# Performance work log

Hardware: AMD Instinct MI355X
Metric: run time of the kernel (lower is better)

Reference implementation:

```python
import jax, jax.numpy as jnp
import numpy as np

HEAD_DIM = 128


def _apply_rotary(x, cos, sin):
    # x: [B, S, H, HD]; cos/sin: [S, HD//2]
    xr = x.reshape(*x.shape[:-1], -1, 2)  # interleaved pairs
    xe, xo = xr[..., 0], xr[..., 1]
    c = cos[None, :, None, :]
    s = sin[None, :, None, :]
    oe = xe * c - xo * s
    oo = xe * s + xo * c
    return jnp.stack([oe, oo], axis=-1).reshape(x.shape)


def setup_inputs() -> dict:
    key = jax.random.key(0)
    ks = jax.random.split(key, 8)
    B, S, D = 2, 1024, 4096
    KVD = 1024  # n_kv_heads * head_dim = 8 * 128
    MAXB, MAXS, KVH, HD = 2, 2048, 8, HEAD_DIM
    theta = 500000.0
    # rotary tables (real/imag of freqs_cis)
    inv = 1.0 / theta ** (np.arange(0, HD, 2)[: HD // 2].astype(np.float32) / HD)
    t = np.arange(S, dtype=np.float32)
    fr = np.outer(t, inv)
    sc = 0.02
    return {
        "x": jax.random.normal(ks[0], (B, S, D), jnp.float32),
        "wq": jax.random.normal(ks[1], (D, D), jnp.float32) * sc,
        "wk": jax.random.normal(ks[2], (D, KVD), jnp.float32) * sc,
        "wv": jax.random.normal(ks[3], (D, KVD), jnp.float32) * sc,
        "wo": jax.random.normal(ks[4], (D, D), jnp.float32) * sc,
        "freqs_cos": jnp.asarray(np.cos(fr)),
        "freqs_sin": jnp.asarray(np.sin(fr)),
        "cache_k": jnp.zeros((MAXB, MAXS, KVH, HD), jnp.float32),
        "cache_v": jnp.zeros((MAXB, MAXS, KVH, HD), jnp.float32),
        "start_pos": 0,
    }


def reference(x, wq, wk, wv, wo, freqs_cos, freqs_sin, cache_k, cache_v, start_pos):
    B, S, D = x.shape
    HD = HEAD_DIM
    H = wq.shape[1] // HD
    KVH = wk.shape[1] // HD
    n_rep = H // KVH

    xq = (x @ wq).reshape(B, S, H, HD)
    xk = (x @ wk).reshape(B, S, KVH, HD)
    xv = (x @ wv).reshape(B, S, KVH, HD)

    xq = _apply_rotary(xq, freqs_cos, freqs_sin)
    xk = _apply_rotary(xk, freqs_cos, freqs_sin)

    # KV-cache update (scatter at start_pos), then read back prefix
    cache_k = cache_k.at[:B, start_pos:start_pos + S].set(xk)
    cache_v = cache_v.at[:B, start_pos:start_pos + S].set(xv)
    keys = cache_k[:B, : start_pos + S]    # [B, T, KVH, HD]
    values = cache_v[:B, : start_pos + S]

    # GQA: repeat kv heads
    keys = jnp.repeat(keys, n_rep, axis=2)      # [B, T, H, HD]
    values = jnp.repeat(values, n_rep, axis=2)

    scale = 1.0 / jnp.sqrt(jnp.float32(HD))
    scores = jnp.einsum("bshd,bthd->bhst", xq, keys) * scale  # [B, H, S, T]

    # causal mask: zeros for the start_pos prefix, upper-triangular -inf after
    T = start_pos + S
    causal = jnp.triu(jnp.full((S, S), -jnp.inf, jnp.float32), k=1)
    mask = jnp.concatenate([jnp.zeros((S, start_pos), jnp.float32), causal], axis=1)  # [S, T]
    scores = scores + mask[None, None, :, :]

    probs = jax.nn.softmax(scores, axis=-1)
    out = jnp.einsum("bhst,bthd->bshd", probs, values).reshape(B, S, D)
    return out @ wo
```

## Files before the change

kernel.cpp:

```cpp
#include <hip/hip_runtime.h>
#include <stdint.h>

#define B_    2
#define S_    1024
#define D_    4096
#define KVD_  1024
#define H_    32
#define KVH_  8
#define HD_   128
#define M_    (B_ * S_)
#define N1_   (D_ + 2 * KVD_)
#define QK_SCALE_L2E (0.08838834764831845f * 1.4426950408889634f)

typedef __attribute__((ext_vector_type(8))) short bf16x8;
typedef __attribute__((ext_vector_type(4))) float f32x4;
typedef __attribute__((ext_vector_type(4))) unsigned short u16x4;
typedef __attribute__((ext_vector_type(8))) unsigned short u16x8;

__device__ inline unsigned short f2bf(float f) {
  unsigned u = __float_as_uint(f);
  u += 0x7FFFu + ((u >> 16) & 1u);
  return (unsigned short)(u >> 16);
}
__device__ inline float bf2f(unsigned short b) {
  return __uint_as_float(((unsigned)b) << 16);
}

#define ASYNC_LD16(g, l) __builtin_amdgcn_global_load_lds( \
    (const __attribute__((address_space(1))) void*)(g),    \
    (__attribute__((address_space(3))) void*)(l), 16, 0, 0)

#define MFMA16(a, b, c) __builtin_amdgcn_mfma_f32_16x16x32_bf16(a, b, c, 0, 0, 0)

#define WAIT_LGKM0() do { asm volatile("s_waitcnt lgkmcnt(0)" ::: "memory"); \
                          __builtin_amdgcn_sched_barrier(0); } while (0)
#define SCHED_PIN() __builtin_amdgcn_sched_barrier(0)
#define BAR() __builtin_amdgcn_s_barrier()

__global__ __launch_bounds__(256) void k_cvt_x(const float* __restrict__ x,
                                               unsigned short* __restrict__ xb) {
  size_t i = ((size_t)blockIdx.x * 256 + threadIdx.x) * 4;
  float4 v = *(const float4*)(x + i);
  u16x4 o;
  o[0] = f2bf(v.x); o[1] = f2bf(v.y); o[2] = f2bf(v.z); o[3] = f2bf(v.w);
  *(u16x4*)(xb + i) = o;
}

__global__ __launch_bounds__(256) void k_transpose_w(const float* __restrict__ in,
                                                     unsigned short* __restrict__ out,
                                                     int R, int C) {
  __shared__ unsigned short tile[64][72];
  int t = threadIdx.x;
  int c0 = blockIdx.x * 64, r0 = blockIdx.y * 64;
#pragma unroll
  for (int j = 0; j < 4; ++j) {
    int r = (t >> 4) + 16 * j;
    int c = (t & 15) * 4;
    float4 v = *(const float4*)(in + (size_t)(r0 + r) * C + c0 + c);
    tile[r][c + 0] = f2bf(v.x); tile[r][c + 1] = f2bf(v.y);
    tile[r][c + 2] = f2bf(v.z); tile[r][c + 3] = f2bf(v.w);
  }
  __syncthreads();
#pragma unroll
  for (int j = 0; j < 2; ++j) {
    int cc = (t >> 3) + 32 * j;
    int r = (t & 7) * 8;
    u16x8 o;
#pragma unroll
    for (int i = 0; i < 8; ++i) o[i] = tile[r + i][cc];
    *(u16x8*)(out + (size_t)(c0 + cc) * R + r0 + r) = o;
  }
}

__global__ __launch_bounds__(512, 2) void k_gemm_g1(const unsigned short* __restrict__ A,
                                                    const unsigned short* __restrict__ Bt,
                                                    unsigned short* __restrict__ C) {
  __shared__ unsigned short L[2 * 28672];
  const int tid = threadIdx.x, lane = tid & 63, w = tid >> 6;
  const int l15 = lane & 15, l4 = lane >> 4;
  const int wm = w >> 2, wn = w & 3;
  const int brow = blockIdx.y * 256, bcol = blockIdx.x * 192;
  const unsigned short* gA = A + (size_t)brow * 4096;
  const unsigned short* gB = Bt + (size_t)bcol * 4096;
  const int srow = lane >> 3;
  const int scol = ((lane & 7) ^ (srow & 7)) * 8;

#define G1_ST_A(buf, kt, r0) ASYNC_LD16( \
    gA + (size_t)((r0) + w * 8 + srow) * 4096 + (kt) * 64 + scol, \
    L + (buf) * 28672 + ((r0) + w * 8) * 64)
#define G1_ST_B(buf, kt, r0) ASYNC_LD16( \
    gB + (size_t)((r0) + w * 8 + srow) * 4096 + (kt) * 64 + scol, \
    L + (buf) * 28672 + 16384 + ((r0) + w * 8) * 64)
#define G1_ST_TILE(buf, kt) do { \
    G1_ST_A(buf, kt, 0); G1_ST_A(buf, kt, 64); G1_ST_A(buf, kt, 128); G1_ST_A(buf, kt, 192); \
    G1_ST_B(buf, kt, 0); G1_ST_B(buf, kt, 64); G1_ST_B(buf, kt, 128); } while (0)

  const int aoff0 = (wm * 128 + l15) * 64 + ((l4 + 0) ^ (l15 & 7)) * 8;
  const int aoff1 = (wm * 128 + l15) * 64 + ((l4 + 4) ^ (l15 & 7)) * 8;
  const int boff0 = 16384 + (wn * 48 + l15) * 64 + ((l4 + 0) ^ (l15 & 7)) * 8;
  const int boff1 = 16384 + (wn * 48 + l15) * 64 + ((l4 + 4) ^ (l15 & 7)) * 8;

  f32x4 acc[8][3] = {};

  G1_ST_TILE(0, 0);
  G1_ST_TILE(1, 1);
  asm volatile("s_waitcnt vmcnt(7)" ::: "memory");
  BAR();

  for (int t = 0; t < 64; ++t) {
    const unsigned short* Lc = L + (t & 1) * 28672;
    bf16x8 af[4], bk[3];

#pragma unroll
    for (int m = 0; m < 4; ++m) af[m] = *(const bf16x8*)(Lc + aoff0 + m * 1024);
#pragma unroll
    for (int n = 0; n < 3; ++n) bk[n] = *(const bf16x8*)(Lc + boff0 + n * 1024);
    SCHED_PIN(); BAR(); WAIT_LGKM0();
    __builtin_amdgcn_s_setprio(1);
#pragma unroll
    for (int m = 0; m < 4; ++m)
#pragma unroll
      for (int n = 0; n < 3; ++n) acc[m][n] = MFMA16(af[m], bk[n], acc[m][n]);
    __builtin_amdgcn_s_setprio(0);
    BAR();

#pragma unroll
    for (int m = 0; m < 4; ++m) af[m] = *(const bf16x8*)(Lc + aoff0 + (m + 4) * 1024);
    SCHED_PIN(); BAR(); WAIT_LGKM0();
    __builtin_amdgcn_s_setprio(1);
#pragma unroll
    for (int m = 0; m < 4; ++m)
#pragma unroll
      for (int n = 0; n < 3; ++n) acc[m + 4][n] = MFMA16(af[m], bk[n], acc[m + 4][n]);
    __builtin_amdgcn_s_setprio(0);
    BAR();

#pragma unroll
    for (int m = 0; m < 4; ++m) af[m] = *(const bf16x8*)(Lc + aoff1 + m * 1024);
#pragma unroll
    for (int n = 0; n < 3; ++n) bk[n] = *(const bf16x8*)(Lc + boff1 + n * 1024);
    SCHED_PIN(); BAR(); WAIT_LGKM0();
    __builtin_amdgcn_s_setprio(1);
#pragma unroll
    for (int m = 0; m < 4; ++m)
#pragma unroll
      for (int n = 0; n < 3; ++n) acc[m][n] = MFMA16(af[m], bk[n], acc[m][n]);
    __builtin_amdgcn_s_setprio(0);
    BAR();

#pragma unroll
    for (int m = 0; m < 4; ++m) af[m] = *(const bf16x8*)(Lc + aoff1 + (m + 4) * 1024);
    SCHED_PIN(); BAR(); WAIT_LGKM0();
    __builtin_amdgcn_s_setprio(1);
#pragma unroll
    for (int m = 0; m < 4; ++m)
#pragma unroll
      for (int n = 0; n < 3; ++n) acc[m + 4][n] = MFMA16(af[m], bk[n], acc[m + 4][n]);
    __builtin_amdgcn_s_setprio(0);
    SCHED_PIN();
    if (t + 2 < 64) {
      G1_ST_TILE(t & 1, t + 2);
      asm volatile("s_waitcnt vmcnt(7)" ::: "memory");
    } else if (t + 1 < 64) {
      asm volatile("s_waitcnt vmcnt(0)" ::: "memory");
    }
    BAR();
  }
#undef G1_ST_TILE
#undef G1_ST_A
#undef G1_ST_B

#pragma unroll
  for (int mf = 0; mf < 8; ++mf)
#pragma unroll
    for (int nf = 0; nf < 3; ++nf)
#pragma unroll
      for (int q = 0; q < 4; ++q) {
        int row = brow + wm * 128 + mf * 16 + l4 * 4 + q;
        int col = bcol + wn * 48 + nf * 16 + l15;
        C[(size_t)row * N1_ + col] = f2bf(acc[mf][nf][q]);
      }
}

__global__ __launch_bounds__(512, 2) void k_gemm_g2(const unsigned short* __restrict__ A,
                                                    const unsigned short* __restrict__ Bt,
                                                    float* __restrict__ C) {
  __shared__ unsigned short L[2 * 24576];
  const int tid = threadIdx.x, lane = tid & 63, w = tid >> 6;
  const int l15 = lane & 15, l4 = lane >> 4;
  const int wm = w >> 2, wn = w & 3;
  const int brow = blockIdx.y * 128, bcol = blockIdx.x * 256;
  const unsigned short* gA = A + (size_t)brow * 4096;
  const unsigned short* gB = Bt + (size_t)bcol * 4096;
  const int srow = lane >> 3;
  const int scol = ((lane & 7) ^ (srow & 7)) * 8;

#define G2_ST_A(buf, kt, r0) ASYNC_LD16( \
    gA + (size_t)((r0) + w * 8 + srow) * 4096 + (kt) * 64 + scol, \
    L + (buf) * 24576 + ((r0) + w * 8) * 64)
#define G2_ST_B(buf, kt, r0) ASYNC_LD16( \
    gB + (size_t)((r0) + w * 8 + srow) * 4096 + (kt) * 64 + scol, \
    L + (buf) * 24576 + 8192 + ((r0) + w * 8) * 64)
#define G2_ST_TILE(buf, kt) do { \
    G2_ST_A(buf, kt, 0); G2_ST_A(buf, kt, 64); \
    G2_ST_B(buf, kt, 0); G2_ST_B(buf, kt, 64); G2_ST_B(buf, kt, 128); G2_ST_B(buf, kt, 192); } while (0)

  const int aoff0 = (wm * 64 + l15) * 64 + ((l4 + 0) ^ (l15 & 7)) * 8;
  const int aoff1 = (wm * 64 + l15) * 64 + ((l4 + 4) ^ (l15 & 7)) * 8;
  const int boff0 = 8192 + (wn * 64 + l15) * 64 + ((l4 + 0) ^ (l15 & 7)) * 8;
  const int boff1 = 8192 + (wn * 64 + l15) * 64 + ((l4 + 4) ^ (l15 & 7)) * 8;

  f32x4 acc[4][4] = {};

  G2_ST_TILE(0, 0);
  G2_ST_TILE(1, 1);
  asm volatile("s_waitcnt vmcnt(6)" ::: "memory");
  BAR();

  for (int t = 0; t < 64; ++t) {
    const unsigned short* Lc = L + (t & 1) * 24576;
    bf16x8 af[4], bk[4];

#pragma unroll
    for (int m = 0; m < 4; ++m) af[m] = *(const bf16x8*)(Lc + aoff0 + m * 1024);
#pragma unroll
    for (int n = 0; n < 4; ++n) bk[n] = *(const bf16x8*)(Lc + boff0 + n * 1024);
    SCHED_PIN(); BAR(); WAIT_LGKM0();
    __builtin_amdgcn_s_setprio(1);
#pragma unroll
    for (int m = 0; m < 4; ++m)
#pragma unroll
      for (int n = 0; n < 4; ++n) acc[m][n] = MFMA16(af[m], bk[n], acc[m][n]);
    __builtin_amdgcn_s_setprio(0);
    BAR();

#pragma unroll
    for (int m = 0; m < 4; ++m) af[m] = *(const bf16x8*)(Lc + aoff1 + m * 1024);
#pragma unroll
    for (int n = 0; n < 4; ++n) bk[n] = *(const bf16x8*)(Lc + boff1 + n * 1024);
    SCHED_PIN(); BAR(); WAIT_LGKM0();
    __builtin_amdgcn_s_setprio(1);
#pragma unroll
    for (int m = 0; m < 4; ++m)
#pragma unroll
      for (int n = 0; n < 4; ++n) acc[m][n] = MFMA16(af[m], bk[n], acc[m][n]);
    __builtin_amdgcn_s_setprio(0);
    SCHED_PIN();
    if (t + 2 < 64) {
      G2_ST_TILE(t & 1, t + 2);
      asm volatile("s_waitcnt vmcnt(6)" ::: "memory");
    } else if (t + 1 < 64) {
      asm volatile("s_waitcnt vmcnt(0)" ::: "memory");
    }
    BAR();
  }
#undef G2_ST_TILE
#undef G2_ST_A
#undef G2_ST_B

#pragma unroll
  for (int mf = 0; mf < 4; ++mf)
#pragma unroll
    for (int nf = 0; nf < 4; ++nf)
#pragma unroll
      for (int q = 0; q < 4; ++q) {
        int row = brow + wm * 64 + mf * 16 + l4 * 4 + q;
        int col = bcol + wn * 64 + nf * 16 + l15;
        C[(size_t)row * D_ + col] = acc[mf][nf][q];
      }
}

__global__ __launch_bounds__(256) void k_rope(unsigned short* __restrict__ qkv,
                                              const float* __restrict__ fc,
                                              const float* __restrict__ fs) {
  int t = blockIdx.y;
  int idx = blockIdx.x * 256 + threadIdx.x;
  int i = idx & 63;
  int hs = idx >> 6;
  int s = t & (S_ - 1);
  int n0 = (hs < H_) ? hs * HD_ : D_ + (hs - H_) * HD_;
  unsigned short* p = qkv + (size_t)t * N1_ + n0 + 2 * i;
  unsigned v = *(const unsigned*)p;
  float xe = bf2f((unsigned short)(v & 0xffff));
  float xo = bf2f((unsigned short)(v >> 16));
  float c = fc[s * 64 + i], sn = fs[s * 64 + i];
  float oe = xe * c - xo * sn;
  float oo = xe * sn + xo * c;
  if (hs < H_) { oe *= QK_SCALE_L2E; oo *= QK_SCALE_L2E; }
  *(unsigned*)p = (unsigned)f2bf(oe) | ((unsigned)f2bf(oo) << 16);
}

__global__ __launch_bounds__(256) void k_transpose_v(const unsigned short* __restrict__ qkv,
                                                     unsigned short* __restrict__ vt) {
  int bh = blockIdx.z;
  int d0 = blockIdx.x * 64;
  int s0 = blockIdx.y * 64;
  __shared__ unsigned short tile[64][72];
  int t = threadIdx.x;
  const unsigned short* src = qkv + (size_t)(bh >> 3) * S_ * N1_ + D_ + KVD_ + (bh & 7) * HD_;
#pragma unroll
  for (int j = 0; j < 2; ++j) {
    int s = (t >> 3) + 32 * j;
    int d = (t & 7) * 8;
    u16x8 v = *(const u16x8*)(src + (size_t)(s0 + s) * N1_ + d0 + d);
#pragma unroll
    for (int i = 0; i < 8; ++i) tile[s][d + i] = v[i];
  }
  __syncthreads();
#pragma unroll
  for (int j = 0; j < 2; ++j) {
    int d = (t >> 3) + 32 * j;
    int s = (t & 7) * 8;
    u16x8 o;
#pragma unroll
    for (int i = 0; i < 8; ++i) o[i] = tile[s + i][d];
    *(u16x8*)(vt + (size_t)(bh * HD_ + d0 + d) * S_ + s0 + s) = o;
  }
}

__global__ __launch_bounds__(256) void k_flash(const unsigned short* __restrict__ qkv,
                                               const unsigned short* __restrict__ vt,
                                               unsigned short* __restrict__ ao) {
  int f = blockIdx.x;
  int bh = f >> 3;
  int qt = (f & 256) ? (7 - (f & 7)) : (f & 7);
  int b = bh >> 5, h = bh & 31;
  int kh = h >> 2;
  int tid = threadIdx.x, lane = tid & 63, w = tid >> 6;
  int l15 = lane & 15, l4 = lane >> 4;

  __shared__ unsigned short Ks[2 * 64 * 128];
  __shared__ unsigned short Vs[2 * 128 * 64];
  __shared__ unsigned short Ps[4][32 * 64];

  int qb0 = qt * 128;
  int rwb = qb0 + w * 32;
  int NT = 2 * qt + 2;

  const unsigned short* qp = qkv + (size_t)(b * S_ + rwb) * N1_ + h * HD_;
  bf16x8 qf[2][4];
#pragma unroll
  for (int qr = 0; qr < 2; ++qr)
#pragma unroll
    for (int ks = 0; ks < 4; ++ks)
      qf[qr][ks] = *(const bf16x8*)(qp + (size_t)(qr * 16 + l15) * N1_ + ks * 32 + l4 * 8);

  f32x4 o[2][8];
#pragma unroll
  for (int qr = 0; qr < 2; ++qr)
#pragma unroll
    for (int d = 0; d < 8; ++d) o[qr][d] = (f32x4){0.f, 0.f, 0.f, 0.f};
  float mrun[2][4], lrun[2][4];
#pragma unroll
  for (int qr = 0; qr < 2; ++qr)
#pragma unroll
    for (int q = 0; q < 4; ++q) { mrun[qr][q] = -1e30f; lrun[qr][q] = 0.f; }

  const unsigned short* kbase = qkv + (size_t)(b * S_) * N1_ + D_ + kh * HD_;
  const unsigned short* vbase = vt + (size_t)(b * KVH_ + kh) * HD_ * S_;
  int krl = lane >> 4, kcu = lane & 15;
  int vrl = lane >> 3, vcu = lane & 7;

#define STAGE_KV(bo, itt) do {                                               \
    int kv0s = (itt) * 64;                                                   \
    _Pragma("unroll")                                                        \
    for (int j = 0; j < 4; ++j) {                                            \
      int kc = w * 4 + j;                                                    \
      int krow = kc * 4 + krl;                                               \
      int su = kcu ^ (krow & 7);                                             \
      ASYNC_LD16(kbase + (size_t)(kv0s + krow) * N1_ + su * 8,               \
                 Ks + (bo) * 8192 + kc * 512);                               \
      int vrow = kc * 8 + vrl;                                               \
      int sv = vcu ^ (vrow & 7);                                             \
      ASYNC_LD16(vbase + (size_t)vrow * S_ + kv0s + sv * 8,                  \
                 Vs + (bo) * 8192 + kc * 512);                               \
    }                                                                        \
  } while (0)

  int cur = 0;
  STAGE_KV(0, 0);

  for (int it = 0; it < NT; ++it) {
    int kv0 = it * 64;
    if (it + 1 < NT) {
      STAGE_KV(cur ^ 1, it + 1);
      asm volatile("s_waitcnt vmcnt(8)" ::: "memory");
    } else {
      asm volatile("s_waitcnt vmcnt(0)" ::: "memory");
    }
    __builtin_amdgcn_s_barrier();
    __builtin_amdgcn_sched_barrier(0);

    if (kv0 <= rwb + 31) {
      const unsigned short* Kc = Ks + cur * 8192;
      const unsigned short* Vc = Vs + cur * 8192;

      f32x4 sf[2][4] = {};
      __builtin_amdgcn_s_setprio(1);
#pragma unroll
      for (int ks = 0; ks < 4; ++ks)
#pragma unroll
        for (int n = 0; n < 4; ++n) {
          int row = n * 16 + l15;
          int u = (l4 + ks * 4) ^ (row & 7);
          bf16x8 kf = *(const bf16x8*)(Kc + row * 128 + u * 8);
          sf[0][n] = MFMA16(qf[0][ks], kf, sf[0][n]);
          sf[1][n] = MFMA16(qf[1][ks], kf, sf[1][n]);
        }
      __builtin_amdgcn_s_setprio(0);

      if (kv0 + 63 > rwb) {
#pragma unroll
        for (int qr = 0; qr < 2; ++qr)
#pragma unroll
          for (int n = 0; n < 4; ++n)
#pragma unroll
            for (int q = 0; q < 4; ++q) {
              int rq = rwb + qr * 16 + l4 * 4 + q;
              int ck = kv0 + n * 16 + l15;
              if (ck > rq) sf[qr][n][q] = -1e30f;
            }
      }

#pragma unroll
      for (int qr = 0; qr < 2; ++qr) {
        float mt[4], rs[4];
#pragma unroll
        for (int q = 0; q < 4; ++q) {
          float m0 = fmaxf(fmaxf(sf[qr][0][q], sf[qr][1][q]),
                           fmaxf(sf[qr][2][q], sf[qr][3][q]));
#pragma unroll
          for (int off = 1; off < 16; off <<= 1) m0 = fmaxf(m0, __shfl_xor(m0, off, 16));
          mt[q] = m0;
        }
        bool grow = (mt[0] > mrun[qr][0]) || (mt[1] > mrun[qr][1]) ||
                    (mt[2] > mrun[qr][2]) || (mt[3] > mrun[qr][3]);
        if (__any(grow)) {
#pragma unroll
          for (int q = 0; q < 4; ++q) {
            float mn = fmaxf(mrun[qr][q], mt[q]);
            float c = __builtin_amdgcn_exp2f(mrun[qr][q] - mn);
            lrun[qr][q] *= c;
            mrun[qr][q] = mn;
#pragma unroll
            for (int d = 0; d < 8; ++d) o[qr][d][q] *= c;
          }
        }
#pragma unroll
        for (int q = 0; q < 4; ++q) rs[q] = 0.f;
#pragma unroll
        for (int n = 0; n < 4; ++n)
#pragma unroll
          for (int q = 0; q < 4; ++q) {
            float p = __builtin_amdgcn_exp2f(sf[qr][n][q] - mrun[qr][q]);
            sf[qr][n][q] = p;
            rs[q] += p;
          }
#pragma unroll
        for (int q = 0; q < 4; ++q) {
#pragma unroll
          for (int off = 1; off < 16; off <<= 1) rs[q] += __shfl_xor(rs[q], off, 16);
          lrun[qr][q] += rs[q];
        }
      }

      unsigned short* pw = Ps[w];
#pragma unroll
      for (int qr = 0; qr < 2; ++qr)
#pragma unroll
        for (int n = 0; n < 4; ++n)
#pragma unroll
          for (int q = 0; q < 4; ++q) {
            int rp = qr * 16 + l4 * 4 + q;
            int cp = n * 16 + l15;
            pw[rp * 64 + (((cp >> 3) ^ (rp & 7)) * 8) + (cp & 7)] = f2bf(sf[qr][n][q]);
          }

      __builtin_amdgcn_s_setprio(1);
#pragma unroll
      for (int kvs = 0; kvs < 2; ++kvs) {
        bf16x8 pa0 = *(const bf16x8*)(pw + (l15) * 64 + (((l4 + kvs * 4) ^ (l15 & 7)) * 8));
        bf16x8 pa1 = *(const bf16x8*)(pw + (16 + l15) * 64 + (((l4 + kvs * 4) ^ (l15 & 7)) * 8));
#pragma unroll
        for (int d = 0; d < 8; ++d) {
          int vrow = d * 16 + l15;
          int u = (l4 + kvs * 4) ^ (vrow & 7);
          bf16x8 vf = *(const bf16x8*)(Vc + vrow * 64 + u * 8);
          o[0][d] = MFMA16(pa0, vf, o[0][d]);
          o[1][d] = MFMA16(pa1, vf, o[1][d]);
        }
      }
      __builtin_amdgcn_s_setprio(0);
    }

    __builtin_amdgcn_s_barrier();
    cur ^= 1;
  }
#undef STAGE_KV

  float invl[2][4];
#pragma unroll
  for (int qr = 0; qr < 2; ++qr)
#pragma unroll
    for (int q = 0; q < 4; ++q) invl[qr][q] = 1.f / lrun[qr][q];
#pragma unroll
  for (int qr = 0; qr < 2; ++qr)
#pragma unroll
    for (int d = 0; d < 8; ++d)
#pragma unroll
      for (int q = 0; q < 4; ++q) {
        int row = b * S_ + rwb + qr * 16 + l4 * 4 + q;
        ao[(size_t)row * D_ + h * HD_ + d * 16 + l15] = f2bf(o[qr][d][q] * invl[qr][q]);
      }
}

extern "C" void kernel_launch(void* const* d_in, const int* in_sizes, int n_in,
                              void* d_out, int out_size, void* d_ws, size_t ws_size,
                              hipStream_t stream) {
  const float* x  = (const float*)d_in[0];
  const float* wq = (const float*)d_in[1];
  const float* wk = (const float*)d_in[2];
  const float* wv = (const float*)d_in[3];
  const float* wo = (const float*)d_in[4];
  const float* fc = (const float*)d_in[5];
  const float* fs = (const float*)d_in[6];
  float* out = (float*)d_out;

  char* ws = (char*)d_ws;
  unsigned short* xb  = (unsigned short*)ws; ws += (size_t)M_ * D_ * 2;
  unsigned short* w1t = (unsigned short*)ws; ws += (size_t)N1_ * D_ * 2;
  unsigned short* wot = (unsigned short*)ws; ws += (size_t)D_ * D_ * 2;
  unsigned short* qkv = (unsigned short*)ws; ws += (size_t)M_ * N1_ * 2;
  unsigned short* vtb = (unsigned short*)ws; ws += (size_t)B_ * KVH_ * HD_ * S_ * 2;
  unsigned short* ao  = (unsigned short*)ws; ws += (size_t)M_ * D_ * 2;

  k_cvt_x<<<(M_ * D_) / 1024, 256, 0, stream>>>(x, xb);
  k_transpose_w<<<dim3(64, 64), 256, 0, stream>>>(wq, w1t, D_, D_);
  k_transpose_w<<<dim3(16, 64), 256, 0, stream>>>(wk, w1t + (size_t)D_ * D_, D_, KVD_);
  k_transpose_w<<<dim3(16, 64), 256, 0, stream>>>(wv, w1t + (size_t)(D_ + KVD_) * D_, D_, KVD_);
  k_transpose_w<<<dim3(64, 64), 256, 0, stream>>>(wo, wot, D_, D_);

  k_gemm_g1<<<dim3(N1_ / 192, M_ / 256), 512, 0, stream>>>(xb, w1t, qkv);

  k_rope<<<dim3(10, M_), 256, 0, stream>>>(qkv, fc, fs);
  k_transpose_v<<<dim3(2, 16, 16), 256, 0, stream>>>(qkv, vtb);
  k_flash<<<dim3(512), 256, 0, stream>>>(qkv, vtb, ao);

  k_gemm_g2<<<dim3(D_ / 256, M_ / 128), 512, 0, stream>>>(ao, wot, out);
}
```

Before: 309.3 us.

## Enlarge QKV GEMM tile to 256x256 with quarter-tile staged prefetch pipeline

The fused QKV projection GEMM moves from 256x192 to 256x256 block tiles, giving each wave a 128x64 sub-tile. The K-loop is restructured into eight phases per pair of K-steps, each loading a quarter-tile of LDS data. Global prefetch of the next tile is interleaved in half-tile chunks between MFMA phases instead of issued all at once. This aims to raise arithmetic intensity and spread memory traffic more evenly across compute. The trade-offs are a larger LDS footprint (128KB per block), higher register pressure, and fewer blocks in the grid.

```diff
diff --git a/kernel.cpp b/kernel.cpp
--- a/kernel.cpp
+++ b/kernel.cpp
@@ -75,109 +75,130 @@
 __global__ __launch_bounds__(512, 2) void k_gemm_g1(const unsigned short* __restrict__ A,
                                                     const unsigned short* __restrict__ Bt,
                                                     unsigned short* __restrict__ C) {
-  __shared__ unsigned short L[2 * 28672];
+  __shared__ unsigned short L[65536];
   const int tid = threadIdx.x, lane = tid & 63, w = tid >> 6;
   const int l15 = lane & 15, l4 = lane >> 4;
   const int wm = w >> 2, wn = w & 3;
-  const int brow = blockIdx.y * 256, bcol = blockIdx.x * 192;
+  const int brow = blockIdx.y * 256, bcol = blockIdx.x * 256;
   const unsigned short* gA = A + (size_t)brow * 4096;
   const unsigned short* gB = Bt + (size_t)bcol * 4096;
-  const int srow = lane >> 3;
-  const int scol = ((lane & 7) ^ (srow & 7)) * 8;
-
-#define G1_ST_A(buf, kt, r0) ASYNC_LD16( \
-    gA + (size_t)((r0) + w * 8 + srow) * 4096 + (kt) * 64 + scol, \
-    L + (buf) * 28672 + ((r0) + w * 8) * 64)
-#define G1_ST_B(buf, kt, r0) ASYNC_LD16( \
-    gB + (size_t)((r0) + w * 8 + srow) * 4096 + (kt) * 64 + scol, \
-    L + (buf) * 28672 + 16384 + ((r0) + w * 8) * 64)
-#define G1_ST_TILE(buf, kt) do { \
-    G1_ST_A(buf, kt, 0); G1_ST_A(buf, kt, 64); G1_ST_A(buf, kt, 128); G1_ST_A(buf, kt, 192); \
-    G1_ST_B(buf, kt, 0); G1_ST_B(buf, kt, 64); G1_ST_B(buf, kt, 128); } while (0)
-
-  const int aoff0 = (wm * 128 + l15) * 64 + ((l4 + 0) ^ (l15 & 7)) * 8;
-  const int aoff1 = (wm * 128 + l15) * 64 + ((l4 + 4) ^ (l15 & 7)) * 8;
-  const int boff0 = 16384 + (wn * 48 + l15) * 64 + ((l4 + 0) ^ (l15 & 7)) * 8;
-  const int boff1 = 16384 + (wn * 48 + l15) * 64 + ((l4 + 4) ^ (l15 & 7)) * 8;
-
-  f32x4 acc[8][3] = {};
-
-  G1_ST_TILE(0, 0);
-  G1_ST_TILE(1, 1);
-  asm volatile("s_waitcnt vmcnt(7)" ::: "memory");
+  const int scol = ((tid & 7) ^ ((tid >> 3) & 7)) * 8;
+
+#define G1_STAGE_A(bb, s, kt) do {                                       \
+    _Pragma("unroll")                                                    \
+    for (int r = 0; r < 2; ++r) {                                        \
+      int grow = r * 128 + (s) * 64 + (tid >> 3);                        \
+      ASYNC_LD16(gA + (size_t)grow * 4096 + (kt) * 64 + scol,            \
+                 L + (bb) + (s) * 8192 + (r * 64 + w * 8) * 64);         \
+    } } while (0)
+#define G1_STAGE_B(bb, s, kt) do {                                       \
+    _Pragma("unroll")                                                    \
+    for (int r = 0; r < 2; ++r) {                                        \
+      int i6 = r * 64 + (tid >> 3);                                      \
+      int grow = ((i6 >> 5) << 6) + (s) * 32 + (i6 & 31);                \
+      ASYNC_LD16(gB + (size_t)grow * 4096 + (kt) * 64 + scol,            \
+                 L + (bb) + 16384 + (s) * 8192 + (r * 64 + w * 8) * 64); \
+    } } while (0)
+
+#define G1_DS_READS(bb, mh, nh) do {                                     \
+    _Pragma("unroll")                                                    \
+    for (int j = 0; j < 4; ++j)                                          \
+      _Pragma("unroll")                                                  \
+      for (int ks = 0; ks < 2; ++ks)                                     \
+        af[j][ks] = *(const bf16x8*)(L + (bb) + (mh) * 8192 +            \
+            (wm * 64 + j * 16 + l15) * 64 + ((ks * 4 + l4) ^ (l15 & 7)) * 8); \
+    _Pragma("unroll")                                                    \
+    for (int jb = 0; jb < 2; ++jb)                                       \
+      _Pragma("unroll")                                                  \
+      for (int ks = 0; ks < 2; ++ks)                                     \
+        bf[jb][ks] = *(const bf16x8*)(L + (bb) + 16384 + (nh) * 8192 +   \
+            (wn * 32 + jb * 16 + l15) * 64 + ((ks * 4 + l4) ^ (l15 & 7)) * 8); \
+    } while (0)
+
+#define G1_MFMA(mh, nh) do {                                             \
+    __builtin_amdgcn_s_setprio(1);                                       \
+    _Pragma("unroll")                                                    \
+    for (int j = 0; j < 4; ++j)                                          \
+      _Pragma("unroll")                                                  \
+      for (int jb = 0; jb < 2; ++jb)                                     \
+        _Pragma("unroll")                                                \
+        for (int ks = 0; ks < 2; ++ks)                                   \
+          acc[(mh) * 4 + j][(nh) * 2 + jb] =                             \
+            MFMA16(af[j][ks], bf[jb][ks], acc[(mh) * 4 + j][(nh) * 2 + jb]); \
+    __builtin_amdgcn_s_setprio(0);                                       \
+    } while (0)
+
+  f32x4 acc[8][4] = {};
+  bf16x8 af[4][2], bf[2][2];
+
+  G1_STAGE_A(0, 0, 0); G1_STAGE_A(0, 1, 0);
+  G1_STAGE_B(0, 0, 0); G1_STAGE_B(0, 1, 0);
+  G1_STAGE_B(32768, 0, 1); G1_STAGE_A(32768, 1, 1);
+  asm volatile("s_waitcnt vmcnt(4)" ::: "memory");
   BAR();
 
-  for (int t = 0; t < 64; ++t) {
-    const unsigned short* Lc = L + (t & 1) * 28672;
-    bf16x8 af[4], bk[3];
-
-#pragma unroll
-    for (int m = 0; m < 4; ++m) af[m] = *(const bf16x8*)(Lc + aoff0 + m * 1024);
-#pragma unroll
-    for (int n = 0; n < 3; ++n) bk[n] = *(const bf16x8*)(Lc + boff0 + n * 1024);
-    SCHED_PIN(); BAR(); WAIT_LGKM0();
-    __builtin_amdgcn_s_setprio(1);
-#pragma unroll
-    for (int m = 0; m < 4; ++m)
-#pragma unroll
-      for (int n = 0; n < 3; ++n) acc[m][n] = MFMA16(af[m], bk[n], acc[m][n]);
-    __builtin_amdgcn_s_setprio(0);
-    BAR();
-
-#pragma unroll
-    for (int m = 0; m < 4; ++m) af[m] = *(const bf16x8*)(Lc + aoff0 + (m + 4) * 1024);
-    SCHED_PIN(); BAR(); WAIT_LGKM0();
-    __builtin_amdgcn_s_setprio(1);
-#pragma unroll
-    for (int m = 0; m < 4; ++m)
-#pragma unroll
-      for (int n = 0; n < 3; ++n) acc[m + 4][n] = MFMA16(af[m], bk[n], acc[m + 4][n]);
-    __builtin_amdgcn_s_setprio(0);
-    BAR();
-
-#pragma unroll
-    for (int m = 0; m < 4; ++m) af[m] = *(const bf16x8*)(Lc + aoff1 + m * 1024);
-#pragma unroll
-    for (int n = 0; n < 3; ++n) bk[n] = *(const bf16x8*)(Lc + boff1 + n * 1024);
-    SCHED_PIN(); BAR(); WAIT_LGKM0();
-    __builtin_amdgcn_s_setprio(1);
-#pragma unroll
-    for (int m = 0; m < 4; ++m)
-#pragma unroll
-      for (int n = 0; n < 3; ++n) acc[m][n] = MFMA16(af[m], bk[n], acc[m][n]);
-    __builtin_amdgcn_s_setprio(0);
-    BAR();
-
-#pragma unroll
-    for (int m = 0; m < 4; ++m) af[m] = *(const bf16x8*)(Lc + aoff1 + (m + 4) * 1024);
-    SCHED_PIN(); BAR(); WAIT_LGKM0();
-    __builtin_amdgcn_s_setprio(1);
-#pragma unroll
-    for (int m = 0; m < 4; ++m)
-#pragma unroll
-      for (int n = 0; n < 3; ++n) acc[m + 4][n] = MFMA16(af[m], bk[n], acc[m + 4][n]);
-    __builtin_amdgcn_s_setprio(0);
+  for (int i = 0; i < 32; ++i) {
+    const int t0 = 2 * i;
+    const bool more = (i + 1 < 32);
+
+    G1_DS_READS(0, 0, 0);
+    G1_STAGE_A(32768, 0, t0 + 1);
+    SCHED_PIN(); BAR(); WAIT_LGKM0();
+    G1_MFMA(0, 0);
+    BAR();
+    G1_DS_READS(0, 1, 0);
+    G1_STAGE_B(32768, 1, t0 + 1);
+    SCHED_PIN(); BAR(); WAIT_LGKM0();
+    G1_MFMA(1, 0);
+    BAR();
+    G1_DS_READS(0, 1, 1);
+    if (more) G1_STAGE_B(0, 0, t0 + 2);
+    SCHED_PIN(); BAR(); WAIT_LGKM0();
+    G1_MFMA(1, 1);
+    BAR();
+    G1_DS_READS(0, 0, 1);
+    if (more) G1_STAGE_A(0, 1, t0 + 2);
+    SCHED_PIN(); BAR(); WAIT_LGKM0();
+    G1_MFMA(0, 1);
+    if (more) { asm volatile("s_waitcnt vmcnt(4)" ::: "memory"); }
+    else      { asm volatile("s_waitcnt vmcnt(0)" ::: "memory"); }
     SCHED_PIN();
-    if (t + 2 < 64) {
-      G1_ST_TILE(t & 1, t + 2);
-      asm volatile("s_waitcnt vmcnt(7)" ::: "memory");
-    } else if (t + 1 < 64) {
-      asm volatile("s_waitcnt vmcnt(0)" ::: "memory");
-    }
-    BAR();
-  }
-#undef G1_ST_TILE
-#undef G1_ST_A
-#undef G1_ST_B
+    BAR();
+    G1_DS_READS(32768, 0, 0);
+    if (more) G1_STAGE_A(0, 0, t0 + 2);
+    SCHED_PIN(); BAR(); WAIT_LGKM0();
+    G1_MFMA(0, 0);
+    BAR();
+    G1_DS_READS(32768, 1, 0);
+    if (more) G1_STAGE_B(0, 1, t0 + 2);
+    SCHED_PIN(); BAR(); WAIT_LGKM0();
+    G1_MFMA(1, 0);
+    BAR();
+    G1_DS_READS(32768, 1, 1);
+    if (more) G1_STAGE_B(32768, 0, t0 + 3);
+    SCHED_PIN(); BAR(); WAIT_LGKM0();
+    G1_MFMA(1, 1);
+    BAR();
+    G1_DS_READS(32768, 0, 1);
+    if (more) G1_STAGE_A(32768, 1, t0 + 3);
+    SCHED_PIN(); BAR(); WAIT_LGKM0();
+    G1_MFMA(0, 1);
+    if (more) { asm volatile("s_waitcnt vmcnt(4)" ::: "memory"); SCHED_PIN(); }
+    BAR();
+  }
+#undef G1_STAGE_A
+#undef G1_STAGE_B
+#undef G1_DS_READS
+#undef G1_MFMA
 
 #pragma unroll
   for (int mf = 0; mf < 8; ++mf)
 #pragma unroll
-    for (int nf = 0; nf < 3; ++nf)
+    for (int nf = 0; nf < 4; ++nf)
 #pragma unroll
       for (int q = 0; q < 4; ++q) {
-        int row = brow + wm * 128 + mf * 16 + l4 * 4 + q;
-        int col = bcol + wn * 48 + nf * 16 + l15;
+        int row = brow + wm * 128 + (mf >> 2) * 64 + (mf & 3) * 16 + l4 * 4 + q;
+        int col = bcol + wn * 64 + (nf >> 1) * 32 + (nf & 1) * 16 + l15;
         C[(size_t)row * N1_ + col] = f2bf(acc[mf][nf][q]);
       }
 }
@@ -540,7 +561,7 @@
   k_transpose_w<<<dim3(16, 64), 256, 0, stream>>>(wv, w1t + (size_t)(D_ + KVD_) * D_, D_, KVD_);
   k_transpose_w<<<dim3(64, 64), 256, 0, stream>>>(wo, wot, D_, D_);
 
-  k_gemm_g1<<<dim3(N1_ / 192, M_ / 256), 512, 0, stream>>>(xb, w1t, qkv);
+  k_gemm_g1<<<dim3(N1_ / 256, M_ / 256), 512, 0, stream>>>(xb, w1t, qkv);
 
   k_rope<<<dim3(10, M_), 256, 0, stream>>>(qkv, fc, fs);
   k_transpose_v<<<dim3(2, 16, 16), 256, 0, stream>>>(qkv, vtb);
```

New measurement: 331.5 us. +7.2%, slower.

## Fuse RoPE into QKV GEMM epilogue, shrink tile, merge weight transposes

Applied to the files above, without the earlier changes.

The QKV GEMM epilogue now applies rotary embedding and the Q scale directly, using a lane shuffle to pair even and odd columns, so the separate k_rope pass over qkv is removed. The GEMM block tile is reduced from 256 to 128 rows with a smaller LDS footprint and a launch bound of 4 blocks per CU, and A and B loads are staged at different points in the loop. This gives a different pipelining schedule and more blocks in flight. The four weight-transpose launches are merged into one kernel to cut launch overhead. The costs are smaller per-block reuse and extra epilogue loads of the cos/sin tables.

```diff
diff --git a/kernel.cpp b/kernel.cpp
--- a/kernel.cpp
+++ b/kernel.cpp
@@ -46,12 +46,22 @@
   *(u16x4*)(xb + i) = o;
 }
 
-__global__ __launch_bounds__(256) void k_transpose_w(const float* __restrict__ in,
-                                                     unsigned short* __restrict__ out,
-                                                     int R, int C) {
+__global__ __launch_bounds__(256) void k_transpose_all(const float* __restrict__ wq,
+                                                       const float* __restrict__ wk,
+                                                       const float* __restrict__ wv,
+                                                       const float* __restrict__ wo,
+                                                       unsigned short* __restrict__ w1t,
+                                                       unsigned short* __restrict__ wot) {
+  int bid = blockIdx.x;
+  const float* in; unsigned short* out; int C, bx, by;
+  if (bid < 4096)      { in = wq; out = w1t;                          C = 4096; bx = bid & 63; by = bid >> 6; }
+  else if (bid < 5120) { bid -= 4096; in = wk; out = w1t + (size_t)D_ * D_;            C = 1024; bx = bid & 15; by = bid >> 4; }
+  else if (bid < 6144) { bid -= 5120; in = wv; out = w1t + (size_t)(D_ + KVD_) * D_;   C = 1024; bx = bid & 15; by = bid >> 4; }
+  else                 { bid -= 6144; in = wo; out = wot;                              C = 4096; bx = bid & 63; by = bid >> 6; }
+  const int R = 4096;
   __shared__ unsigned short tile[64][72];
   int t = threadIdx.x;
-  int c0 = blockIdx.x * 64, r0 = blockIdx.y * 64;
+  int c0 = bx * 64, r0 = by * 64;
 #pragma unroll
   for (int j = 0; j < 4; ++j) {
     int r = (t >> 4) + 16 * j;
@@ -72,113 +82,110 @@
   }
 }
 
-__global__ __launch_bounds__(512, 2) void k_gemm_g1(const unsigned short* __restrict__ A,
+__global__ __launch_bounds__(512, 4) void k_gemm_g1(const unsigned short* __restrict__ A,
                                                     const unsigned short* __restrict__ Bt,
-                                                    unsigned short* __restrict__ C) {
-  __shared__ unsigned short L[2 * 28672];
+                                                    unsigned short* __restrict__ C,
+                                                    const float* __restrict__ fc,
+                                                    const float* __restrict__ fs) {
+  __shared__ unsigned short L[40960];
   const int tid = threadIdx.x, lane = tid & 63, w = tid >> 6;
   const int l15 = lane & 15, l4 = lane >> 4;
   const int wm = w >> 2, wn = w & 3;
-  const int brow = blockIdx.y * 256, bcol = blockIdx.x * 192;
+  const int brow = blockIdx.y * 128, bcol = blockIdx.x * 192;
   const unsigned short* gA = A + (size_t)brow * 4096;
   const unsigned short* gB = Bt + (size_t)bcol * 4096;
-  const int srow = lane >> 3;
-  const int scol = ((lane & 7) ^ (srow & 7)) * 8;
-
-#define G1_ST_A(buf, kt, r0) ASYNC_LD16( \
-    gA + (size_t)((r0) + w * 8 + srow) * 4096 + (kt) * 64 + scol, \
-    L + (buf) * 28672 + ((r0) + w * 8) * 64)
-#define G1_ST_B(buf, kt, r0) ASYNC_LD16( \
-    gB + (size_t)((r0) + w * 8 + srow) * 4096 + (kt) * 64 + scol, \
-    L + (buf) * 28672 + 16384 + ((r0) + w * 8) * 64)
-#define G1_ST_TILE(buf, kt) do { \
-    G1_ST_A(buf, kt, 0); G1_ST_A(buf, kt, 64); G1_ST_A(buf, kt, 128); G1_ST_A(buf, kt, 192); \
-    G1_ST_B(buf, kt, 0); G1_ST_B(buf, kt, 64); G1_ST_B(buf, kt, 128); } while (0)
-
-  const int aoff0 = (wm * 128 + l15) * 64 + ((l4 + 0) ^ (l15 & 7)) * 8;
-  const int aoff1 = (wm * 128 + l15) * 64 + ((l4 + 4) ^ (l15 & 7)) * 8;
-  const int boff0 = 16384 + (wn * 48 + l15) * 64 + ((l4 + 0) ^ (l15 & 7)) * 8;
-  const int boff1 = 16384 + (wn * 48 + l15) * 64 + ((l4 + 4) ^ (l15 & 7)) * 8;
-
-  f32x4 acc[8][3] = {};
-
-  G1_ST_TILE(0, 0);
-  G1_ST_TILE(1, 1);
-  asm volatile("s_waitcnt vmcnt(7)" ::: "memory");
+  const int scol = ((lane & 7) ^ (lane >> 3)) * 8;
+
+#define G1_ST_A(bb, kt, r) ASYNC_LD16( \
+    gA + (size_t)((r) * 64 + w * 8 + (lane >> 3)) * 4096 + (kt) * 64 + scol, \
+    L + (bb) + ((r) * 64 + w * 8) * 64)
+#define G1_ST_B(bb, kt, r) ASYNC_LD16( \
+    gB + (size_t)((r) * 64 + w * 8 + (lane >> 3)) * 4096 + (kt) * 64 + scol, \
+    L + (bb) + 8192 + ((r) * 64 + w * 8) * 64)
+
+  f32x4 acc[4][3] = {};
+  bf16x8 bfr[3][2], af[2][2];
+
+  G1_ST_A(0, 0, 0); G1_ST_A(0, 0, 1);
+  G1_ST_B(0, 0, 0); G1_ST_B(0, 0, 1); G1_ST_B(0, 0, 2);
+  G1_ST_B(20480, 1, 0); G1_ST_B(20480, 1, 1); G1_ST_B(20480, 1, 2);
+  asm volatile("s_waitcnt vmcnt(3)" ::: "memory");
+  SCHED_PIN();
   BAR();
 
   for (int t = 0; t < 64; ++t) {
-    const unsigned short* Lc = L + (t & 1) * 28672;
-    bf16x8 af[4], bk[3];
-
-#pragma unroll
-    for (int m = 0; m < 4; ++m) af[m] = *(const bf16x8*)(Lc + aoff0 + m * 1024);
-#pragma unroll
-    for (int n = 0; n < 3; ++n) bk[n] = *(const bf16x8*)(Lc + boff0 + n * 1024);
+    const int cb = (t & 1) * 20480, nb = cb ^ 20480;
+
+#pragma unroll
+    for (int nf = 0; nf < 3; ++nf)
+#pragma unroll
+      for (int ks = 0; ks < 2; ++ks)
+        bfr[nf][ks] = *(const bf16x8*)(L + cb + 8192 +
+            (wn * 48 + nf * 16 + l15) * 64 + ((ks * 4 + l4) ^ (l15 & 7)) * 8);
+#pragma unroll
+    for (int i = 0; i < 2; ++i)
+#pragma unroll
+      for (int ks = 0; ks < 2; ++ks)
+        af[i][ks] = *(const bf16x8*)(L + cb +
+            (wm * 64 + i * 16 + l15) * 64 + ((ks * 4 + l4) ^ (l15 & 7)) * 8);
+    if (t + 1 < 64) { G1_ST_A(nb, t + 1, 0); G1_ST_A(nb, t + 1, 1); }
     SCHED_PIN(); BAR(); WAIT_LGKM0();
     __builtin_amdgcn_s_setprio(1);
 #pragma unroll
-    for (int m = 0; m < 4; ++m)
-#pragma unroll
-      for (int n = 0; n < 3; ++n) acc[m][n] = MFMA16(af[m], bk[n], acc[m][n]);
+    for (int i = 0; i < 2; ++i)
+#pragma unroll
+      for (int nf = 0; nf < 3; ++nf)
+#pragma unroll
+        for (int ks = 0; ks < 2; ++ks)
+          acc[i][nf] = MFMA16(af[i][ks], bfr[nf][ks], acc[i][nf]);
     __builtin_amdgcn_s_setprio(0);
     BAR();
 
 #pragma unroll
-    for (int m = 0; m < 4; ++m) af[m] = *(const bf16x8*)(Lc + aoff0 + (m + 4) * 1024);
+    for (int i = 0; i < 2; ++i)
+#pragma unroll
+      for (int ks = 0; ks < 2; ++ks)
+        af[i][ks] = *(const bf16x8*)(L + cb +
+            (wm * 64 + (2 + i) * 16 + l15) * 64 + ((ks * 4 + l4) ^ (l15 & 7)) * 8);
+    if (t + 2 < 64) { G1_ST_B(cb, t + 2, 0); G1_ST_B(cb, t + 2, 1); G1_ST_B(cb, t + 2, 2); }
     SCHED_PIN(); BAR(); WAIT_LGKM0();
     __builtin_amdgcn_s_setprio(1);
 #pragma unroll
-    for (int m = 0; m < 4; ++m)
-#pragma unroll
-      for (int n = 0; n < 3; ++n) acc[m + 4][n] = MFMA16(af[m], bk[n], acc[m + 4][n]);
+    for (int i = 0; i < 2; ++i)
+#pragma unroll
+      for (int nf = 0; nf < 3; ++nf)
+#pragma unroll
+        for (int ks = 0; ks < 2; ++ks)
+          acc[2 + i][nf] = MFMA16(af[i][ks], bfr[nf][ks], acc[2 + i][nf]);
     __builtin_amdgcn_s_setprio(0);
+    if (t + 2 < 64) { asm volatile("s_waitcnt vmcnt(3)" ::: "memory"); }
+    else            { asm volatile("s_waitcnt vmcnt(0)" ::: "memory"); }
+    SCHED_PIN();
     BAR();
-
-#pragma unroll
-    for (int m = 0; m < 4; ++m) af[m] = *(const bf16x8*)(Lc + aoff1 + m * 1024);
-#pragma unroll
-    for (int n = 0; n < 3; ++n) bk[n] = *(const bf16x8*)(Lc + boff1 + n * 1024);
-    SCHED_PIN(); BAR(); WAIT_LGKM0();
-    __builtin_amdgcn_s_setprio(1);
-#pragma unroll
-    for (int m = 0; m < 4; ++m)
-#pragma unroll
-      for (int n = 0; n < 3; ++n) acc[m][n] = MFMA16(af[m], bk[n], acc[m][n]);
-    __builtin_amdgcn_s_setprio(0);
-    BAR();
-
-#pragma unroll
-    for (int m = 0; m < 4; ++m) af[m] = *(const bf16x8*)(Lc + aoff1 + (m + 4) * 1024);
-    SCHED_PIN(); BAR(); WAIT_LGKM0();
-    __builtin_amdgcn_s_setprio(1);
-#pragma unroll
-    for (int m = 0; m < 4; ++m)
-#pragma unroll
-      for (int n = 0; n < 3; ++n) acc[m + 4][n] = MFMA16(af[m], bk[n], acc[m + 4][n]);
-    __builtin_amdgcn_s_setprio(0);
-    SCHED_PIN();
-    if (t + 2 < 64) {
-      G1_ST_TILE(t & 1, t + 2);
-      asm volatile("s_waitcnt vmcnt(7)" ::: "memory");
-    } else if (t + 1 < 64) {
-      asm volatile("s_waitcnt vmcnt(0)" ::: "memory");
-    }
-    BAR();
-  }
-#undef G1_ST_TILE
+  }
 #undef G1_ST_A
 #undef G1_ST_B
 
 #pragma unroll
-  for (int mf = 0; mf < 8; ++mf)
+  for (int mf = 0; mf < 4; ++mf)
 #pragma unroll
     for (int nf = 0; nf < 3; ++nf)
 #pragma unroll
       for (int q = 0; q < 4; ++q) {
-        int row = brow + wm * 128 + mf * 16 + l4 * 4 + q;
+        int row = brow + wm * 64 + mf * 16 + l4 * 4 + q;
         int col = bcol + wn * 48 + nf * 16 + l15;
-        C[(size_t)row * N1_ + col] = f2bf(acc[mf][nf][q]);
+        float v = acc[mf][nf][q];
+        float p = __shfl_xor(v, 1);
+        float r;
+        if (col < D_ + KVD_) {
+          int i = (col & 127) >> 1, s = row & (S_ - 1);
+          float c = fc[s * 64 + i], sn = fs[s * 64 + i];
+          bool ev = (col & 1) == 0;
+          float xe = ev ? v : p, xo = ev ? p : v;
+          r = ev ? (xe * c - xo * sn) : (xe * sn + xo * c);
+          if (col < D_) r *= QK_SCALE_L2E;
+        } else r = v;
+        C[(size_t)row * N1_ + col] = f2bf(r);
       }
 }
 
@@ -268,26 +275,6 @@
         int col = bcol + wn * 64 + nf * 16 + l15;
         C[(size_t)row * D_ + col] = acc[mf][nf][q];
       }
-}
-
-__global__ __launch_bounds__(256) void k_rope(unsigned short* __restrict__ qkv,
-                                              const float* __restrict__ fc,
-                                              const float* __restrict__ fs) {
-  int t = blockIdx.y;
-  int idx = blockIdx.x * 256 + threadIdx.x;
-  int i = idx & 63;
-  int hs = idx >> 6;
-  int s = t & (S_ - 1);
-  int n0 = (hs < H_) ? hs * HD_ : D_ + (hs - H_) * HD_;
-  unsigned short* p = qkv + (size_t)t * N1_ + n0 + 2 * i;
-  unsigned v = *(const unsigned*)p;
-  float xe = bf2f((unsigned short)(v & 0xffff));
-  float xo = bf2f((unsigned short)(v >> 16));
-  float c = fc[s * 64 + i], sn = fs[s * 64 + i];
-  float oe = xe * c - xo * sn;
-  float oo = xe * sn + xo * c;
-  if (hs < H_) { oe *= QK_SCALE_L2E; oo *= QK_SCALE_L2E; }
-  *(unsigned*)p = (unsigned)f2bf(oe) | ((unsigned)f2bf(oo) << 16);
 }
 
 __global__ __launch_bounds__(256) void k_transpose_v(const unsigned short* __restrict__ qkv,
@@ -535,14 +522,10 @@
   unsigned short* ao  = (unsigned short*)ws; ws += (size_t)M_ * D_ * 2;
 
   k_cvt_x<<<(M_ * D_) / 1024, 256, 0, stream>>>(x, xb);
-  k_transpose_w<<<dim3(64, 64), 256, 0, stream>>>(wq, w1t, D_, D_);
-  k_transpose_w<<<dim3(16, 64), 256, 0, stream>>>(wk, w1t + (size_t)D_ * D_, D_, KVD_);
-  k_transpose_w<<<dim3(16, 64), 256, 0, stream>>>(wv, w1t + (size_t)(D_ + KVD_) * D_, D_, KVD_);
-  k_transpose_w<<<dim3(64, 64), 256, 0, stream>>>(wo, wot, D_, D_);
-
-  k_gemm_g1<<<dim3(N1_ / 192, M_ / 256), 512, 0, stream>>>(xb, w1t, qkv);
-
-  k_rope<<<dim3(10, M_), 256, 0, stream>>>(qkv, fc, fs);
+  k_transpose_all<<<10240, 256, 0, stream>>>(wq, wk, wv, wo, w1t, wot);
+
+  k_gemm_g1<<<dim3(N1_ / 192, M_ / 128), 512, 0, stream>>>(xb, w1t, qkv, fc, fs);
+
   k_transpose_v<<<dim3(2, 16, 16), 256, 0, stream>>>(qkv, vtb);
   k_flash<<<dim3(512), 256, 0, stream>>>(qkv, vtb, ao);
 
```

New measurement: 294.0 us. 5.0% less time.
